# Performance work log

Measured on AMD Instinct MI355X. Metric: run time of the kernel, lower is better.

## Reference

```python
import jax, jax.numpy as jnp
import numpy as np

N_FFT = 256
HOP = 64
K = 2       # top-k experts
E = 8       # num experts


def conv1d(x, w, b, stride, pad):
    # x: [B, Cin, L], w: [Cout, Cin, Kw]
    y = jax.lax.conv_general_dilated(x, w, (stride,), [(pad, pad)],
                                     dimension_numbers=('NCH', 'OIH', 'NCH'))
    return y + b[None, :, None]


def stft_mag(x):
    # torch.stft(center=True, pad_mode='reflect', hann window, onesided)
    pad = N_FFT // 2
    xp = jnp.pad(x, ((0, 0), (pad, pad)), mode='reflect')
    n_frames = 1 + (xp.shape[1] - N_FFT) // HOP
    idx = jnp.arange(n_frames)[:, None] * HOP + jnp.arange(N_FFT)[None, :]
    win = 0.5 - 0.5 * jnp.cos(2.0 * jnp.pi * jnp.arange(N_FFT) / N_FFT)  # periodic hann
    frames = xp[:, idx] * win            # [B, F, n_fft]
    return jnp.abs(jnp.fft.rfft(frames, axis=-1))  # [B, F, n_fft//2+1]


def expert_fwd(x, wa3, ba3, wb3, bb3, wa5, ba5, wb5, bb5, wa7, ba7, wb7, bb7):
    # MultiScalePyramidBranch: 3 parallel conv branches (k=3/5/7), 2 conv layers each
    xc = x[:, None, :]  # [B, 1, L]
    outs = []
    for wa, ba, wb, bb in ((wa3, ba3, wb3, bb3), (wa5, ba5, wb5, bb5), (wa7, ba7, wb7, bb7)):
        h = jax.nn.relu(conv1d(xc, wa, ba, 2, wa.shape[-1] // 2))
        h = jax.nn.relu(conv1d(h, wb, bb, 2, 1))
        outs.append(h)
    return jnp.concatenate(outs, axis=1)  # [B, 192, L//4]


def moe_forward(x, Wg1, bg1, Wg2, bg2, Wg3, bg3, ew):
    # gating on frequency domain (stft is computed under no_grad in the original)
    mag = stft_mag(jax.lax.stop_gradient(x))
    pooled = mag.mean(axis=1)                     # adaptive_avg_pool1d(.,1) over frames
    h = jax.nn.relu(pooled @ Wg1 + bg1)
    h = jax.nn.relu(h @ Wg2 + bg2)
    logits = h @ Wg3 + bg3                        # [B, E]
    vals, inds = jax.lax.top_k(logits, K)
    w = jax.nn.softmax(vals, axis=1)              # softmax over the top-k weights
    # vectorized dispatch: run all experts on the whole batch, then gather+combine
    all_out = jax.vmap(expert_fwd, in_axes=(None,) + (0,) * 12)(x, *ew)  # [E, B, C, T]
    B = x.shape[0]
    bidx = jnp.arange(B)
    out = jnp.zeros_like(all_out[0])
    for j in range(K):
        out = out + w[:, j, None, None] * all_out[inds[:, j], bidx]
    return out


def setup_inputs() -> dict:
    key = jax.random.key(0)
    ks = jax.random.split(key, 20)

    def p(k, shape, s=0.02):
        return (s * jax.random.normal(k, shape)).astype(jnp.float32)

    inp = {'x': jax.random.normal(ks[0], (64, 4096), dtype=jnp.float32)}
    inp['Wg1'] = p(ks[1], (129, 256)); inp['bg1'] = jnp.zeros((256,), jnp.float32)
    inp['Wg2'] = p(ks[2], (256, 128)); inp['bg2'] = jnp.zeros((128,), jnp.float32)
    inp['Wg3'] = p(ks[3], (128, E));   inp['bg3'] = jnp.zeros((E,), jnp.float32)
    i = 4
    for ksz in (3, 5, 7):
        inp['wa%d' % ksz] = p(ks[i], (E, 64, 1, ksz)); i += 1
        inp['ba%d' % ksz] = jnp.zeros((E, 64), jnp.float32)
        inp['wb%d' % ksz] = p(ks[i], (E, 64, 64, 3)); i += 1
        inp['bb%d' % ksz] = jnp.zeros((E, 64), jnp.float32)
    return inp


def reference(x, Wg1, bg1, Wg2, bg2, Wg3, bg3,
              wa3, ba3, wb3, bb3, wa5, ba5, wb5, bb5, wa7, ba7, wb7, bb7):
    ew = (wa3, ba3, wb3, bb3, wa5, ba5, wb5, bb5, wa7, ba7, wb7, bb7)
    return moe_forward(x, Wg1, bg1, Wg2, bg2, Wg3, bg3, ew)
```

## Files before the change

kernel.cpp:

```cpp
#include <hip/hip_runtime.h>
#include <math.h>

#define NFFT 256
#define NBINS 129
#define HOP 64
#define NFRAMES 65
#define NB 64
#define LX 4096
#define LH 2048
#define LY 1024
#define NCH 64
#define NBR 3
#define NE 8

#define PART_STRIDE 132
#define PART_BYTES (NB * NFRAMES * PART_STRIDE * 4)
#define WTF_OFF 2197504
#define WTF_PER 98304
#define IW_OFF 2787328

typedef __attribute__((ext_vector_type(8))) short short8;
typedef __attribute__((ext_vector_type(4))) float floatx4;

__device__ __forceinline__ unsigned short bf16r(float f) {
    unsigned u = __builtin_bit_cast(unsigned, f);
    u += 0x7FFFu + ((u >> 16) & 1u);
    return (unsigned short)(u >> 16);
}

__global__ __launch_bounds__(128) void stft_kernel(
    const float* __restrict__ x, float* __restrict__ part) {
    __shared__ float xw[NFFT];
    const int f = blockIdx.x, b = blockIdx.y;
    const int tid = threadIdx.x;

    for (int n = tid; n < NFFT; n += 128) {
        float a2 = (float)(2.0 * 3.14159265358979323846 / 256.0) * (float)n;
        float sn, cn;
        sincosf(a2, &sn, &cn);
        float win = 0.5f - 0.5f * cn;
        int q = f * HOP + n - 128;
        int xi = q < 0 ? -q : (q >= LX ? (2 * LX - 2 - q) : q);
        xw[n] = x[b * LX + xi] * win;
    }
    __syncthreads();

    const int k = tid;
    float ang = (float)(2.0 * 3.14159265358979323846 / 256.0) * (float)k;
    float s1, c1;
    sincosf(ang, &s1, &c1);

    float A0 = 0.f, B0 = 0.f, A1 = 0.f, B1 = 0.f;
    float A2 = 0.f, B2 = 0.f, A3 = 0.f, B3 = 0.f;
    float c0 = 1.f, s0 = 0.f, cc1 = 1.f, ss1 = 0.f;
    float cc2 = 1.f, ss2 = 0.f, cc3 = 1.f, ss3 = 0.f;
    float rNe = 0.f, rNo = 0.f;

#pragma unroll 4
    for (int mq = 0; mq < 16; ++mq) {
        float4 v0 = *(const float4*)&xw[4 * mq];
        float4 v1 = *(const float4*)&xw[64 + 4 * mq];
        float4 v2 = *(const float4*)&xw[128 + 4 * mq];
        float4 v3 = *(const float4*)&xw[192 + 4 * mq];
        float e0[4] = {v0.x, v0.y, v0.z, v0.w};
        float e1[4] = {v1.x, v1.y, v1.z, v1.w};
        float e2[4] = {v2.x, v2.y, v2.z, v2.w};
        float e3[4] = {v3.x, v3.y, v3.z, v3.w};
#pragma unroll
        for (int mm = 0; mm < 4; ++mm) {
            float t;
            A0 = fmaf(e0[mm], c0, A0);  B0 = fmaf(e0[mm], s0, B0);
            A1 = fmaf(e1[mm], cc1, A1); B1 = fmaf(e1[mm], ss1, B1);
            A2 = fmaf(e2[mm], cc2, A2); B2 = fmaf(e2[mm], ss2, B2);
            A3 = fmaf(e3[mm], cc3, A3); B3 = fmaf(e3[mm], ss3, B3);
            if ((mm & 1) == 0) rNe += e0[mm] + e1[mm] + e2[mm] + e3[mm];
            else               rNo += e0[mm] + e1[mm] + e2[mm] + e3[mm];
            t = c0 * c1 - s0 * s1;   s0 = fmaf(c0, s1, s0 * c1);   c0 = t;
            t = cc1 * c1 - ss1 * s1; ss1 = fmaf(cc1, s1, ss1 * c1); cc1 = t;
            t = cc2 * c1 - ss2 * s1; ss2 = fmaf(cc2, s1, ss2 * c1); cc2 = t;
            t = cc3 * c1 - ss3 * s1; ss3 = fmaf(cc3, s1, ss3 * c1); cc3 = t;
        }
    }

    float re = A0, im = B0;
    float Aj[3] = {A1, A2, A3};
    float Bj[3] = {B1, B2, B3};
#pragma unroll
    for (int j = 1; j < 4; ++j) {
        int ph = (j * k) & 3;
        float cf = (ph == 0) ? 1.f : (ph == 2) ? -1.f : 0.f;
        float sf = (ph == 1) ? 1.f : (ph == 3) ? -1.f : 0.f;
        re += cf * Aj[j - 1] - sf * Bj[j - 1];
        im += sf * Aj[j - 1] + cf * Bj[j - 1];
    }

    float* prow = part + (b * NFRAMES + f) * PART_STRIDE;
    prow[k] = sqrtf(re * re + im * im);
    if (tid == 0) prow[128] = fabsf(rNe - rNo);
}

__global__ __launch_bounds__(256) void gating_kernel(
    const float* __restrict__ part,
    const float* __restrict__ Wg1, const float* __restrict__ bg1,
    const float* __restrict__ Wg2, const float* __restrict__ bg2,
    const float* __restrict__ Wg3, const float* __restrict__ bg3,
    const float* __restrict__ wb3, const float* __restrict__ wb5,
    const float* __restrict__ wb7, unsigned short* __restrict__ wTf,
    int* __restrict__ inds, float* __restrict__ wts) {
    __shared__ float pl[NBINS];
    __shared__ float h1[256];
    __shared__ float h2[128];
    __shared__ float lg[NE];
    const int b = blockIdx.x, tid = threadIdx.x;

    for (int fi = b * 256 + tid; fi < 3 * WTF_PER; fi += NB * 256) {
        int br = fi / WTF_PER, r = fi % WTF_PER;
        int e = r / 12288;
        int r2 = r % 12288;
        int mw = r2 / 3072;
        int r3 = r2 % 3072;
        int i = r3 / 1024;
        int r4 = r3 % 1024;
        int kb = r4 / 512;
        int r5 = r4 % 512;
        int lane = r5 / 8, j = r5 % 8;
        int c2 = mw * 16 + (lane & 15);
        int cl = kb * 32 + (lane >> 4) * 8 + j;
        const float* src = (br == 0) ? wb3 : (br == 1) ? wb5 : wb7;
        wTf[fi] = bf16r(src[((e * 64 + c2) * 64 + cl) * 3 + i]);
    }

    if (tid < NBINS) {
        float s = 0.f;
        for (int f = 0; f < NFRAMES; ++f)
            s += part[(b * NFRAMES + f) * PART_STRIDE + tid];
        pl[tid] = s * (1.0f / (float)NFRAMES);
    }
    __syncthreads();
    {
        float s = bg1[tid];
        for (int kk = 0; kk < NBINS; ++kk) s += pl[kk] * Wg1[kk * 256 + tid];
        h1[tid] = fmaxf(s, 0.f);
    }
    __syncthreads();
    if (tid < 128) {
        float s = bg2[tid];
        for (int kk = 0; kk < 256; ++kk) s += h1[kk] * Wg2[kk * 128 + tid];
        h2[tid] = fmaxf(s, 0.f);
    }
    __syncthreads();
    if (tid < NE) {
        float s = bg3[tid];
        for (int kk = 0; kk < 128; ++kk) s += h2[kk] * Wg3[kk * NE + tid];
        lg[tid] = s;
    }
    __syncthreads();
    if (tid == 0) {
        int i0 = 0;
        float v0 = lg[0];
        for (int i = 1; i < NE; ++i)
            if (lg[i] > v0) { v0 = lg[i]; i0 = i; }
        int i1 = -1;
        float v1 = -3.0e38f;
        for (int i = 0; i < NE; ++i) {
            if (i == i0) continue;
            if (lg[i] > v1) { v1 = lg[i]; i1 = i; }
        }
        float e1 = expf(v1 - v0);
        float w0 = 1.f / (1.f + e1);
        inds[b * 2 + 0] = i0;
        inds[b * 2 + 1] = i1;
        wts[b * 2 + 0] = w0;
        wts[b * 2 + 1] = e1 * w0;
    }
}

#define UT 128
#define HPR 68
#define HROWS 258

template <int KSZ>
__device__ __forceinline__ void phaseA_rows(
    const float* __restrict__ xp, const float* wr, float bv, short* hp,
    int tb, int nrow, int t0, int x0) {
    const int lane_cl = threadIdx.x & 63;
    int base = x0 + 8 * tb;
    float xr[16];
    if (base >= 0 && base + 15 < LX) {
#pragma unroll
        for (int ii = 0; ii < 16; ++ii) xr[ii] = xp[base + ii];
    } else {
#pragma unroll
        for (int ii = 0; ii < 16; ++ii) {
            int xi = base + ii;
            xr[ii] = (xi >= 0 && xi < LX) ? xp[xi] : 0.f;
        }
    }
#pragma unroll
    for (int m = 0; m < 4; ++m) {
        if (m >= nrow) break;
        int tl = 4 * tb + m;
        int t = t0 + tl;
        float s = bv;
#pragma unroll
        for (int i = 0; i < KSZ; ++i) s += wr[i] * xr[2 * m + i];
        float h = (t >= 0 && t < LH) ? fmaxf(s, 0.f) : 0.f;
        hp[tl * HPR + lane_cl] = (short)bf16r(h);
    }
}

template <int KSZ>
__device__ __attribute__((always_inline)) void expert_body(
    const float* __restrict__ x,
    const float* __restrict__ wa, const float* __restrict__ ba,
    const float* __restrict__ bb, const unsigned short* __restrict__ wTfbr,
    const int* __restrict__ inds, const float* __restrict__ wts,
    float* __restrict__ out, int br, short* hp) {
    const int u0 = blockIdx.x * UT;
    const int b = blockIdx.z;
    const int tid = threadIdx.x;
    const int lane = tid & 63;
    const int quad = lane >> 4;
    const int l15 = lane & 15;
    const int wv = __builtin_amdgcn_readfirstlane(tid >> 6);
    const int mw = wv & 3;
    const int nh = wv >> 2;
    const int pad = KSZ >> 1;
    const int t0 = 2 * u0 - 1;
    const int x0 = 2 * t0 - pad;

    const float* xp = x + b * LX;

    float fin[4][4];
#pragma unroll
    for (int q = 0; q < 4; ++q)
#pragma unroll
        for (int r = 0; r < 4; ++r) fin[q][r] = 0.f;

#pragma unroll 1
    for (int slot = 0; slot < 2; ++slot) {
        const int e = __builtin_amdgcn_readfirstlane(inds[b * 2 + slot]);
        const float wj = wts[b * 2 + slot];

        float wr[KSZ];
#pragma unroll
        for (int i = 0; i < KSZ; ++i) wr[i] = wa[(e * NCH + lane) * KSZ + i];
        const float bv = ba[e * NCH + lane];

        __syncthreads();

#pragma unroll 2
        for (int it = 0; it < 8; ++it)
            phaseA_rows<KSZ>(xp, wr, bv, hp, wv + 8 * it, 4, t0, x0);
        if (wv == 0)
            phaseA_rows<KSZ>(xp, wr, bv, hp, 64, 2, t0, x0);
        __syncthreads();

        float br4[4];
#pragma unroll
        for (int r = 0; r < 4; ++r)
            br4[r] = bb[e * NCH + mw * 16 + quad * 4 + r];

        short8 af[3][2];
        {
            const unsigned short* wbase =
                wTfbr + e * 12288 + mw * 3072 + lane * 8;
#pragma unroll
            for (int i = 0; i < 3; ++i)
#pragma unroll
                for (int kb = 0; kb < 2; ++kb)
                    af[i][kb] = *(const short8*)&wbase[i * 1024 + kb * 512];
        }

#pragma unroll 2
        for (int q = 0; q < 4; ++q) {
            int nt = nh * 4 + q;
            int nb = nt * 16 + l15;
            floatx4 acc = {br4[0], br4[1], br4[2], br4[3]};
#pragma unroll
            for (int i = 0; i < 3; ++i) {
                int tl = 2 * nb + i;
#pragma unroll
                for (int kb = 0; kb < 2; ++kb) {
                    int sb = tl * HPR + kb * 32 + quad * 8;
                    union { short8 v; unsigned long long q2[2]; } B;
                    B.q2[0] = *(const unsigned long long*)&hp[sb];
                    B.q2[1] = *(const unsigned long long*)&hp[sb + 4];
                    acc = __builtin_amdgcn_mfma_f32_16x16x32_bf16(
                        af[i][kb], B.v, acc, 0, 0, 0);
                }
            }
#pragma unroll
            for (int r = 0; r < 4; ++r)
                fin[q][r] += wj * fmaxf(acc[r], 0.f);
        }
    }

#pragma unroll
    for (int q = 0; q < 4; ++q) {
        int u = u0 + (nh * 4 + q) * 16 + l15;
#pragma unroll
        for (int r = 0; r < 4; ++r) {
            int c2 = mw * 16 + quad * 4 + r;
            out[(long)(b * 192 + br * 64 + c2) * LY + u] = fin[q][r];
        }
    }
}

__global__ __launch_bounds__(512, 2) void expert_kernel(
    const float* __restrict__ x,
    const float* __restrict__ wa3, const float* __restrict__ ba3,
    const float* __restrict__ bb3,
    const float* __restrict__ wa5, const float* __restrict__ ba5,
    const float* __restrict__ bb5,
    const float* __restrict__ wa7, const float* __restrict__ ba7,
    const float* __restrict__ bb7,
    const unsigned short* __restrict__ wTf,
    const int* __restrict__ inds, const float* __restrict__ wts,
    float* __restrict__ out) {
    __shared__ short hp[HROWS * HPR];

    const int br = blockIdx.y;
    if (br == 0)
        expert_body<3>(x, wa3, ba3, bb3, wTf, inds, wts, out, 0, hp);
    else if (br == 1)
        expert_body<5>(x, wa5, ba5, bb5, wTf + WTF_PER, inds, wts, out, 1, hp);
    else
        expert_body<7>(x, wa7, ba7, bb7, wTf + 2 * WTF_PER, inds, wts, out, 2, hp);
}

extern "C" void kernel_launch(void* const* d_in, const int* in_sizes, int n_in,
                              void* d_out, int out_size, void* d_ws, size_t ws_size,
                              hipStream_t stream) {
    const float* x   = (const float*)d_in[0];
    const float* Wg1 = (const float*)d_in[1];
    const float* bg1 = (const float*)d_in[2];
    const float* Wg2 = (const float*)d_in[3];
    const float* bg2 = (const float*)d_in[4];
    const float* Wg3 = (const float*)d_in[5];
    const float* bg3 = (const float*)d_in[6];
    const float* wa3 = (const float*)d_in[7];
    const float* ba3 = (const float*)d_in[8];
    const float* wb3 = (const float*)d_in[9];
    const float* bb3 = (const float*)d_in[10];
    const float* wa5 = (const float*)d_in[11];
    const float* ba5 = (const float*)d_in[12];
    const float* wb5 = (const float*)d_in[13];
    const float* bb5 = (const float*)d_in[14];
    const float* wa7 = (const float*)d_in[15];
    const float* ba7 = (const float*)d_in[16];
    const float* wb7 = (const float*)d_in[17];
    const float* bb7 = (const float*)d_in[18];

    float* part = (float*)d_ws;
    unsigned short* wTf = (unsigned short*)((char*)d_ws + WTF_OFF);
    int* inds = (int*)((char*)d_ws + IW_OFF);
    float* wts = (float*)((char*)d_ws + IW_OFF + 512);

    stft_kernel<<<dim3(NFRAMES, NB), 128, 0, stream>>>(x, part);
    gating_kernel<<<NB, 256, 0, stream>>>(part, Wg1, bg1, Wg2, bg2, Wg3, bg3,
                                          wb3, wb5, wb7, wTf, inds, wts);
    expert_kernel<<<dim3(LY / UT, NBR, NB), 512, 0, stream>>>(
        x, wa3, ba3, bb3, wa5, ba5, bb5, wa7, ba7, bb7, wTf,
        inds, wts, (float*)d_out);
}
```

Baseline: 185.0 us.

## Move weight repack into STFT kernel and compute both experts' first layer together

The bf16 repack of the second-layer expert weights moves from the serial 64-block gating kernel into the wide STFT kernel, where each of the 4160 blocks converts one 128-element chunk. The expert kernel now computes the first conv layer for both selected experts in one pass, sharing the x loads and dropping one pair of barriers. Each result goes into its own LDS buffer. This doubles LDS use per block (about 70KB), which may limit the two-blocks-per-CU occupancy the launch bounds request.

```diff
diff --git a/kernel.cpp b/kernel.cpp
--- a/kernel.cpp
+++ b/kernel.cpp
@@ -14,7 +14,6 @@
 #define NE 8
 
 #define PART_STRIDE 132
-#define PART_BYTES (NB * NFRAMES * PART_STRIDE * 4)
 #define WTF_OFF 2197504
 #define WTF_PER 98304
 #define IW_OFF 2787328
@@ -29,10 +28,33 @@
 }
 
 __global__ __launch_bounds__(128) void stft_kernel(
-    const float* __restrict__ x, float* __restrict__ part) {
+    const float* __restrict__ x,
+    const float* __restrict__ wb3, const float* __restrict__ wb5,
+    const float* __restrict__ wb7, unsigned short* __restrict__ wTf,
+    float* __restrict__ part) {
     __shared__ float xw[NFFT];
     const int f = blockIdx.x, b = blockIdx.y;
     const int tid = threadIdx.x;
+
+    {
+        int fi = (b * NFRAMES + f) * 128 + tid;
+        if (fi < 3 * WTF_PER) {
+            int br = fi / WTF_PER, r = fi % WTF_PER;
+            int e = r / 12288;
+            int r2 = r % 12288;
+            int mw = r2 / 3072;
+            int r3 = r2 % 3072;
+            int i = r3 / 1024;
+            int r4 = r3 % 1024;
+            int kb = r4 / 512;
+            int r5 = r4 % 512;
+            int lane = r5 / 8, j = r5 % 8;
+            int c2 = mw * 16 + (lane & 15);
+            int cl = kb * 32 + (lane >> 4) * 8 + j;
+            const float* src = (br == 0) ? wb3 : (br == 1) ? wb5 : wb7;
+            wTf[fi] = bf16r(src[((e * 64 + c2) * 64 + cl) * 3 + i]);
+        }
+    }
 
     for (int n = tid; n < NFFT; n += 128) {
         float a2 = (float)(2.0 * 3.14159265358979323846 / 256.0) * (float)n;
@@ -104,31 +126,12 @@
     const float* __restrict__ Wg1, const float* __restrict__ bg1,
     const float* __restrict__ Wg2, const float* __restrict__ bg2,
     const float* __restrict__ Wg3, const float* __restrict__ bg3,
-    const float* __restrict__ wb3, const float* __restrict__ wb5,
-    const float* __restrict__ wb7, unsigned short* __restrict__ wTf,
     int* __restrict__ inds, float* __restrict__ wts) {
     __shared__ float pl[NBINS];
     __shared__ float h1[256];
     __shared__ float h2[128];
     __shared__ float lg[NE];
     const int b = blockIdx.x, tid = threadIdx.x;
-
-    for (int fi = b * 256 + tid; fi < 3 * WTF_PER; fi += NB * 256) {
-        int br = fi / WTF_PER, r = fi % WTF_PER;
-        int e = r / 12288;
-        int r2 = r % 12288;
-        int mw = r2 / 3072;
-        int r3 = r2 % 3072;
-        int i = r3 / 1024;
-        int r4 = r3 % 1024;
-        int kb = r4 / 512;
-        int r5 = r4 % 512;
-        int lane = r5 / 8, j = r5 % 8;
-        int c2 = mw * 16 + (lane & 15);
-        int cl = kb * 32 + (lane >> 4) * 8 + j;
-        const float* src = (br == 0) ? wb3 : (br == 1) ? wb5 : wb7;
-        wTf[fi] = bf16r(src[((e * 64 + c2) * 64 + cl) * 3 + i]);
-    }
 
     if (tid < NBINS) {
         float s = 0.f;
@@ -180,42 +183,12 @@
 #define HROWS 258
 
 template <int KSZ>
-__device__ __forceinline__ void phaseA_rows(
-    const float* __restrict__ xp, const float* wr, float bv, short* hp,
-    int tb, int nrow, int t0, int x0) {
-    const int lane_cl = threadIdx.x & 63;
-    int base = x0 + 8 * tb;
-    float xr[16];
-    if (base >= 0 && base + 15 < LX) {
-#pragma unroll
-        for (int ii = 0; ii < 16; ++ii) xr[ii] = xp[base + ii];
-    } else {
-#pragma unroll
-        for (int ii = 0; ii < 16; ++ii) {
-            int xi = base + ii;
-            xr[ii] = (xi >= 0 && xi < LX) ? xp[xi] : 0.f;
-        }
-    }
-#pragma unroll
-    for (int m = 0; m < 4; ++m) {
-        if (m >= nrow) break;
-        int tl = 4 * tb + m;
-        int t = t0 + tl;
-        float s = bv;
-#pragma unroll
-        for (int i = 0; i < KSZ; ++i) s += wr[i] * xr[2 * m + i];
-        float h = (t >= 0 && t < LH) ? fmaxf(s, 0.f) : 0.f;
-        hp[tl * HPR + lane_cl] = (short)bf16r(h);
-    }
-}
-
-template <int KSZ>
 __device__ __attribute__((always_inline)) void expert_body(
     const float* __restrict__ x,
     const float* __restrict__ wa, const float* __restrict__ ba,
     const float* __restrict__ bb, const unsigned short* __restrict__ wTfbr,
     const int* __restrict__ inds, const float* __restrict__ wts,
-    float* __restrict__ out, int br, short* hp) {
+    float* __restrict__ out, int br, short* hp0, short* hp1) {
     const int u0 = blockIdx.x * UT;
     const int b = blockIdx.z;
     const int tid = threadIdx.x;
@@ -231,6 +204,73 @@
 
     const float* xp = x + b * LX;
 
+    const int e0 = __builtin_amdgcn_readfirstlane(inds[b * 2 + 0]);
+    const int e1 = __builtin_amdgcn_readfirstlane(inds[b * 2 + 1]);
+    const float wj0 = wts[b * 2 + 0];
+    const float wj1 = wts[b * 2 + 1];
+
+    float wr0[KSZ], wr1[KSZ];
+#pragma unroll
+    for (int i = 0; i < KSZ; ++i) {
+        wr0[i] = wa[(e0 * NCH + lane) * KSZ + i];
+        wr1[i] = wa[(e1 * NCH + lane) * KSZ + i];
+    }
+    const float bv0 = ba[e0 * NCH + lane];
+    const float bv1 = ba[e1 * NCH + lane];
+
+#pragma unroll 2
+    for (int it = 0; it < 8; ++it) {
+        int tb = wv + 8 * it;
+        int base = x0 + 8 * tb;
+        float xr[16];
+        if (base >= 0 && base + 15 < LX) {
+#pragma unroll
+            for (int ii = 0; ii < 16; ++ii) xr[ii] = xp[base + ii];
+        } else {
+#pragma unroll
+            for (int ii = 0; ii < 16; ++ii) {
+                int xi = base + ii;
+                xr[ii] = (xi >= 0 && xi < LX) ? xp[xi] : 0.f;
+            }
+        }
+#pragma unroll
+        for (int m = 0; m < 4; ++m) {
+            int tl = 4 * tb + m;
+            int t = t0 + tl;
+            float s0v = bv0, s1v = bv1;
+#pragma unroll
+            for (int i = 0; i < KSZ; ++i) {
+                s0v = fmaf(wr0[i], xr[2 * m + i], s0v);
+                s1v = fmaf(wr1[i], xr[2 * m + i], s1v);
+            }
+            bool ok = (t >= 0 && t < LH);
+            float h0 = ok ? fmaxf(s0v, 0.f) : 0.f;
+            float h1 = ok ? fmaxf(s1v, 0.f) : 0.f;
+            hp0[tl * HPR + lane] = (short)bf16r(h0);
+            hp1[tl * HPR + lane] = (short)bf16r(h1);
+        }
+    }
+    if (wv == 0) {
+#pragma unroll
+        for (int m = 0; m < 2; ++m) {
+            int tl = 256 + m;
+            int t = t0 + tl;
+            int xb = x0 + 2 * tl;
+            float s0v = bv0, s1v = bv1;
+#pragma unroll
+            for (int i = 0; i < KSZ; ++i) {
+                int xi = xb + i;
+                float xvv = (xi >= 0 && xi < LX) ? xp[xi] : 0.f;
+                s0v = fmaf(wr0[i], xvv, s0v);
+                s1v = fmaf(wr1[i], xvv, s1v);
+            }
+            bool ok = (t >= 0 && t < LH);
+            hp0[tl * HPR + lane] = (short)bf16r(ok ? fmaxf(s0v, 0.f) : 0.f);
+            hp1[tl * HPR + lane] = (short)bf16r(ok ? fmaxf(s1v, 0.f) : 0.f);
+        }
+    }
+    __syncthreads();
+
     float fin[4][4];
 #pragma unroll
     for (int q = 0; q < 4; ++q)
@@ -239,22 +279,9 @@
 
 #pragma unroll 1
     for (int slot = 0; slot < 2; ++slot) {
-        const int e = __builtin_amdgcn_readfirstlane(inds[b * 2 + slot]);
-        const float wj = wts[b * 2 + slot];
-
-        float wr[KSZ];
-#pragma unroll
-        for (int i = 0; i < KSZ; ++i) wr[i] = wa[(e * NCH + lane) * KSZ + i];
-        const float bv = ba[e * NCH + lane];
-
-        __syncthreads();
-
-#pragma unroll 2
-        for (int it = 0; it < 8; ++it)
-            phaseA_rows<KSZ>(xp, wr, bv, hp, wv + 8 * it, 4, t0, x0);
-        if (wv == 0)
-            phaseA_rows<KSZ>(xp, wr, bv, hp, 64, 2, t0, x0);
-        __syncthreads();
+        const int e = slot ? e1 : e0;
+        const float wj = slot ? wj1 : wj0;
+        const short* hp = slot ? hp1 : hp0;
 
         float br4[4];
 #pragma unroll
@@ -318,15 +345,18 @@
     const unsigned short* __restrict__ wTf,
     const int* __restrict__ inds, const float* __restrict__ wts,
     float* __restrict__ out) {
-    __shared__ short hp[HROWS * HPR];
+    __shared__ short hp0[HROWS * HPR];
+    __shared__ short hp1[HROWS * HPR];
 
     const int br = blockIdx.y;
     if (br == 0)
-        expert_body<3>(x, wa3, ba3, bb3, wTf, inds, wts, out, 0, hp);
+        expert_body<3>(x, wa3, ba3, bb3, wTf, inds, wts, out, 0, hp0, hp1);
     else if (br == 1)
-        expert_body<5>(x, wa5, ba5, bb5, wTf + WTF_PER, inds, wts, out, 1, hp);
+        expert_body<5>(x, wa5, ba5, bb5, wTf + WTF_PER, inds, wts, out, 1,
+                       hp0, hp1);
     else
-        expert_body<7>(x, wa7, ba7, bb7, wTf + 2 * WTF_PER, inds, wts, out, 2, hp);
+        expert_body<7>(x, wa7, ba7, bb7, wTf + 2 * WTF_PER, inds, wts, out, 2,
+                       hp0, hp1);
 }
 
 extern "C" void kernel_launch(void* const* d_in, const int* in_sizes, int n_in,
@@ -357,9 +387,10 @@
     int* inds = (int*)((char*)d_ws + IW_OFF);
     float* wts = (float*)((char*)d_ws + IW_OFF + 512);
 
-    stft_kernel<<<dim3(NFRAMES, NB), 128, 0, stream>>>(x, part);
+    stft_kernel<<<dim3(NFRAMES, NB), 128, 0, stream>>>(x, wb3, wb5, wb7, wTf,
+                                                       part);
     gating_kernel<<<NB, 256, 0, stream>>>(part, Wg1, bg1, Wg2, bg2, Wg3, bg3,
-                                          wb3, wb5, wb7, wTf, inds, wts);
+                                          inds, wts);
     expert_kernel<<<dim3(LY / UT, NBR, NB), 512, 0, stream>>>(
         x, wa3, ba3, bb3, wa5, ba5, bb5, wa7, ba7, bb7, wTf,
         inds, wts, (float*)d_out);
```

Measured after the change: 177.2 us. -4.2%, faster.
